# Kernel tuning notes

Measured on AMD Instinct MI355X. Metric: run time of the kernel, lower is better.

Reference implementation:

```python
import jax, jax.numpy as jnp
import numpy as np

WS = (7, 7)          # window size
N = WS[0] * WS[1]    # 49 tokens per window
C = 128              # dim
H = 4                # num heads
D = C // H           # head dim = 32
B = 8192             # batch * num_windows
NW = 1024            # windows per image
SCALE = D ** -0.5


def _relative_position_index():
    coords_h = np.arange(WS[0])
    coords_w = np.arange(WS[1])
    coords = np.stack(np.meshgrid(coords_h, coords_w, indexing='ij'))  # [2,Wh,Ww]
    flat = coords.reshape(2, -1)                                        # [2,N]
    rel = flat[:, :, None] - flat[:, None, :]                           # [2,N,N]
    rel = rel.transpose(1, 2, 0).astype(np.int64)                       # [N,N,2]
    rel[:, :, 0] += WS[0] - 1
    rel[:, :, 1] += WS[1] - 1
    rel[:, :, 0] *= 2 * WS[1] - 1
    return rel.sum(-1)                                                  # [N,N]


def setup_inputs() -> dict:
    key = jax.random.key(0)
    ks = jax.random.split(key, 8)
    s = 0.02
    return {
        'x': jax.random.normal(ks[0], (B, N, C), jnp.float32),
        'y': jax.random.normal(ks[1], (B, N, C), jnp.float32),
        'mask': jnp.zeros((NW, N, N), jnp.float32),
        'Wq': jax.random.normal(ks[2], (C, C), jnp.float32) * s,
        'bq': jnp.zeros((C,), jnp.float32),
        'Wkv': jax.random.normal(ks[3], (C, 2 * C), jnp.float32) * s,
        'bkv': jnp.zeros((2 * C,), jnp.float32),
        'bias_table': jax.random.normal(ks[4], ((2 * WS[0] - 1) * (2 * WS[1] - 1), H), jnp.float32) * s,
        'Wp': jax.random.normal(ks[5], (C, C), jnp.float32) * s,
        'bp': jnp.zeros((C,), jnp.float32),
        'rel_idx': jnp.asarray(_relative_position_index(), jnp.int32),
    }


def reference(x, y, mask, Wq, bq, Wkv, bkv, bias_table, Wp, bp, rel_idx):
    b = x.shape[0]
    # q/kv projections
    q = (x @ Wq + bq).reshape(b, N, H, D).transpose(0, 2, 1, 3) * SCALE   # [B,H,N,D]
    kv = (y @ Wkv + bkv).reshape(b, N, 2, H, D).transpose(2, 0, 3, 1, 4)  # [2,B,H,N,D]
    k, v = kv[0], kv[1]
    attn = jnp.einsum('bhnd,bhmd->bhnm', q, k)                            # [B,H,N,N]
    # relative position bias gather
    bias = bias_table[rel_idx.reshape(-1)].reshape(N, N, H).transpose(2, 0, 1)  # [H,N,N]
    attn = attn + bias[None]
    # mask add per window
    nW = mask.shape[0]
    attn = attn.reshape(b // nW, nW, H, N, N) + mask[None, :, None]
    attn = attn.reshape(b, H, N, N)
    attn = jax.nn.softmax(attn, axis=-1)
    out = jnp.einsum('bhnm,bhmd->bhnd', attn, v)                          # [B,H,N,D]
    out = out.transpose(0, 2, 1, 3).reshape(b, N, C)
    return out @ Wp + bp
```

## Files before the change

### kernel.cpp

```cpp
#include <hip/hip_runtime.h>
#include <cstddef>


#define MFMA16 __builtin_amdgcn_mfma_f32_16x16x32_bf16

typedef float f32x4 __attribute__((ext_vector_type(4)));
typedef __bf16 bf16x8 __attribute__((ext_vector_type(8)));
typedef unsigned short u16x8 __attribute__((ext_vector_type(8)));

constexpr int NTOK = 49;
constexpr int CDIM = 128;
constexpr int NWIN = 1024;
constexpr int NB = 8192;
constexpr float SCALE_F = 0.17677669529663687f;

__device__ __forceinline__ unsigned short f2bf(float f) {
  unsigned int u = __builtin_bit_cast(unsigned int, f);
  u += 0x7FFFu + ((u >> 16) & 1u);
  return (unsigned short)(u >> 16);
}

__device__ __forceinline__ int sw128(int row, int col) {
  return (row << 8) + ((((col >> 3) ^ row) & 15) << 4) + ((col & 7) << 1);
}
__device__ __forceinline__ int sw64(int row, int col) {
  return (row << 7) + ((((col >> 3) ^ (row >> 1)) & 7) << 4) + ((col & 7) << 1);
}

__global__ void prepack_kernel(const float* __restrict__ Wq, const float* __restrict__ Wkv,
                               const float* __restrict__ Wp, const float* __restrict__ bias_table,
                               const int* __restrict__ rel_idx,
                               unsigned short* __restrict__ wFrag, float* __restrict__ wBias) {
  int t = blockIdx.x * 256 + threadIdx.x;
  if (t < 8192) {
    const int mat = t >> 11;
    const int g = t & 2047;
    const int frag = g >> 6, lane = g & 63;
    const int nt = frag >> 2, ks = frag & 3;
    const int li = lane & 15, q4 = lane >> 4;
    const int n = nt * 16 + li;
    u16x8 tmp;
#pragma unroll
    for (int j = 0; j < 8; ++j) {
      const int k = ks * 32 + q4 * 8 + j;
      float v;
      if (mat == 0) v = Wq[k * 128 + n];
      else if (mat == 1) v = Wkv[k * 256 + n];
      else if (mat == 2) v = Wkv[k * 256 + 128 + n];
      else v = Wp[k * 128 + n];
      tmp[j] = f2bf(v);
    }
    *(u16x8*)(wFrag + (size_t)t * 8) = tmp;
  } else {
    const int tb = t - 8192;
    if (tb < 2401) {
      const int r = rel_idx[tb];
#pragma unroll
      for (int h = 0; h < 4; ++h) wBias[h * 2401 + tb] = bias_table[r * 4 + h];
    }
  }
}

__global__ __launch_bounds__(256, 3) void attn_kernel(
    const float* __restrict__ x, const float* __restrict__ y, const float* __restrict__ mask,
    const float* __restrict__ bq, const float* __restrict__ bkv, const float* __restrict__ bp,
    const unsigned short* __restrict__ wFrag, const float* __restrict__ wBias,
    float* __restrict__ out) {
  __shared__ __align__(16) unsigned char lds[49152];
  const int tid = threadIdx.x;
  const int w = tid >> 6;
  const int lane = tid & 63;
  const int li = lane & 15;
  const int q4 = lane >> 4;
  const int b = blockIdx.x;
  const int mh = w >> 1;
  const int nh = w & 1;

  bf16x8 ax[2][4], ay[2][4];
#pragma unroll
  for (int t = 0; t < 2; ++t) {
    const int mrow = mh * 32 + t * 16 + li;
    const bool mv = mrow < NTOK;
    const float* xr = x + ((size_t)b * NTOK + (mv ? mrow : 0)) * CDIM;
    const float* yr = y + ((size_t)b * NTOK + (mv ? mrow : 0)) * CDIM;
#pragma unroll
    for (int ks = 0; ks < 4; ++ks) {
      const int c0 = ks * 32 + q4 * 8;
      float4 a0 = *(const float4*)(xr + c0);
      float4 a1 = *(const float4*)(xr + c0 + 4);
      float4 b0 = *(const float4*)(yr + c0);
      float4 b1 = *(const float4*)(yr + c0 + 4);
      if (!mv) {
        a0.x = a0.y = a0.z = a0.w = 0.f; a1.x = a1.y = a1.z = a1.w = 0.f;
        b0.x = b0.y = b0.z = b0.w = 0.f; b1.x = b1.y = b1.z = b1.w = 0.f;
      }
      u16x8 ta, tb;
      ta[0] = f2bf(a0.x); ta[1] = f2bf(a0.y); ta[2] = f2bf(a0.z); ta[3] = f2bf(a0.w);
      ta[4] = f2bf(a1.x); ta[5] = f2bf(a1.y); ta[6] = f2bf(a1.z); ta[7] = f2bf(a1.w);
      tb[0] = f2bf(b0.x); tb[1] = f2bf(b0.y); tb[2] = f2bf(b0.z); tb[3] = f2bf(b0.w);
      tb[4] = f2bf(b1.x); tb[5] = f2bf(b1.y); tb[6] = f2bf(b1.z); tb[7] = f2bf(b1.w);
      ax[t][ks] = __builtin_bit_cast(bf16x8, ta);
      ay[t][ks] = __builtin_bit_cast(bf16x8, tb);
    }
  }

  const unsigned short* wq = wFrag + 0 * 16384 + nh * 8192;
  const unsigned short* wk = wFrag + 1 * 16384 + nh * 8192;
  const unsigned short* wv = wFrag + 2 * 16384 + nh * 8192;
  const unsigned short* wp = wFrag + 3 * 16384 + nh * 8192;

#pragma unroll
  for (int ntl = 0; ntl < 4; ++ntl) {
    bf16x8 wf[4];
#pragma unroll
    for (int ks = 0; ks < 4; ++ks)
      wf[ks] = *(const bf16x8*)(wq + (ntl * 4 + ks) * 512 + lane * 8);
    const int n = nh * 64 + ntl * 16 + li;
    const float bv = bq[n];
#pragma unroll
    for (int t = 0; t < 2; ++t) {
      f32x4 acc = {0.f, 0.f, 0.f, 0.f};
#pragma unroll
      for (int ks = 0; ks < 4; ++ks) acc = MFMA16(ax[t][ks], wf[ks], acc, 0, 0, 0);
#pragma unroll
      for (int r = 0; r < 4; ++r) {
        const int m = mh * 32 + t * 16 + q4 * 4 + r;
        *(unsigned short*)(lds + sw128(m, n)) = f2bf(acc[r] + bv);
      }
    }
  }
#pragma unroll
  for (int ntl = 0; ntl < 4; ++ntl) {
    bf16x8 wf[4];
#pragma unroll
    for (int ks = 0; ks < 4; ++ks)
      wf[ks] = *(const bf16x8*)(wk + (ntl * 4 + ks) * 512 + lane * 8);
    const int n = nh * 64 + ntl * 16 + li;
    const float bv = bkv[n];
#pragma unroll
    for (int t = 0; t < 2; ++t) {
      f32x4 acc = {0.f, 0.f, 0.f, 0.f};
#pragma unroll
      for (int ks = 0; ks < 4; ++ks) acc = MFMA16(ay[t][ks], wf[ks], acc, 0, 0, 0);
#pragma unroll
      for (int r = 0; r < 4; ++r) {
        const int m = mh * 32 + t * 16 + q4 * 4 + r;
        *(unsigned short*)(lds + 16384 + sw128(m, n)) = f2bf(acc[r] + bv);
      }
    }
  }
#pragma unroll
  for (int ntl = 0; ntl < 4; ++ntl) {
    bf16x8 wf[4];
#pragma unroll
    for (int ks = 0; ks < 4; ++ks)
      wf[ks] = *(const bf16x8*)(wv + (ntl * 4 + ks) * 512 + lane * 8);
    const int n = nh * 64 + ntl * 16 + li;
    const float bv = bkv[128 + n];
#pragma unroll
    for (int t = 0; t < 2; ++t) {
      f32x4 acc = {0.f, 0.f, 0.f, 0.f};
#pragma unroll
      for (int ks = 0; ks < 4; ++ks) acc = MFMA16(ay[t][ks], wf[ks], acc, 0, 0, 0);
#pragma unroll
      for (int r = 0; r < 4; ++r) {
        const int m = mh * 32 + t * 16 + q4 * 4 + r;
        *(unsigned short*)(lds + 32768 + sw64(n, m)) = f2bf(acc[r] + bv);
      }
    }
  }
  __syncthreads();

  const int h = w;
  const int PS = h * 8192;
  f32x4 s[4][4];
  {
    bf16x8 aq[4], bk[4];
#pragma unroll
    for (int mt = 0; mt < 4; ++mt)
      aq[mt] = *(const bf16x8*)(lds + sw128(mt * 16 + li, h * 32 + q4 * 8));
#pragma unroll
    for (int nt = 0; nt < 4; ++nt)
      bk[nt] = *(const bf16x8*)(lds + 16384 + sw128(nt * 16 + li, h * 32 + q4 * 8));
    const f32x4 zz = {0.f, 0.f, 0.f, 0.f};
#pragma unroll
    for (int mt = 0; mt < 4; ++mt)
#pragma unroll
      for (int nt = 0; nt < 4; ++nt) s[mt][nt] = MFMA16(aq[mt], bk[nt], zz, 0, 0, 0);
  }
  const float* __restrict__ maskw = mask + (size_t)(b & (NWIN - 1)) * 2401;
  const float* __restrict__ biash = wBias + h * 2401;
#pragma unroll
  for (int mt = 0; mt < 4; ++mt) {
#pragma unroll
    for (int r = 0; r < 4; ++r) {
      const int m = mt * 16 + q4 * 4 + r;
      const bool mvld = m < NTOK;
      const int mo = (mvld ? m : 0) * NTOK;
      float vv[4];
#pragma unroll
      for (int nt = 0; nt < 4; ++nt) {
        const int n = nt * 16 + li;
        float t = SCALE_F * s[mt][nt][r];
        if (n < NTOK) {
          if (mvld) t += biash[mo + n] + maskw[mo + n];
        } else {
          t = -1e30f;
        }
        vv[nt] = t;
      }
      float mx = fmaxf(fmaxf(vv[0], vv[1]), fmaxf(vv[2], vv[3]));
      mx = fmaxf(mx, __shfl_xor(mx, 1, 16));
      mx = fmaxf(mx, __shfl_xor(mx, 2, 16));
      mx = fmaxf(mx, __shfl_xor(mx, 4, 16));
      mx = fmaxf(mx, __shfl_xor(mx, 8, 16));
      float sm = 0.f;
#pragma unroll
      for (int nt = 0; nt < 4; ++nt) {
        vv[nt] = __expf(vv[nt] - mx);
        sm += vv[nt];
      }
      sm += __shfl_xor(sm, 1, 16);
      sm += __shfl_xor(sm, 2, 16);
      sm += __shfl_xor(sm, 4, 16);
      sm += __shfl_xor(sm, 8, 16);
      const float inv = __builtin_amdgcn_rcpf(sm);
#pragma unroll
      for (int nt = 0; nt < 4; ++nt) s[mt][nt][r] = vv[nt] * inv;
    }
  }
  __syncthreads();
#pragma unroll
  for (int mt = 0; mt < 4; ++mt)
#pragma unroll
    for (int r = 0; r < 4; ++r) {
      const int m = mt * 16 + q4 * 4 + r;
#pragma unroll
      for (int nt = 0; nt < 4; ++nt)
        *(unsigned short*)(lds + PS + sw64(m, nt * 16 + li)) = f2bf(s[mt][nt][r]);
    }

  f32x4 o[4][2];
  {
    bf16x8 ap[4][2], bv2[2][2];
#pragma unroll
    for (int mt = 0; mt < 4; ++mt)
#pragma unroll
      for (int ks = 0; ks < 2; ++ks)
        ap[mt][ks] = *(const bf16x8*)(lds + PS + sw64(mt * 16 + li, ks * 32 + q4 * 8));
#pragma unroll
    for (int nti = 0; nti < 2; ++nti)
#pragma unroll
      for (int ks = 0; ks < 2; ++ks)
        bv2[nti][ks] =
            *(const bf16x8*)(lds + 32768 + sw64(h * 32 + nti * 16 + li, ks * 32 + q4 * 8));
#pragma unroll
    for (int mt = 0; mt < 4; ++mt)
#pragma unroll
      for (int nti = 0; nti < 2; ++nti) {
        f32x4 acc = {0.f, 0.f, 0.f, 0.f};
#pragma unroll
        for (int ks = 0; ks < 2; ++ks) acc = MFMA16(ap[mt][ks], bv2[nti][ks], acc, 0, 0, 0);
        o[mt][nti] = acc;
      }
  }
  __syncthreads();

#pragma unroll
  for (int mt = 0; mt < 4; ++mt)
#pragma unroll
    for (int nti = 0; nti < 2; ++nti)
#pragma unroll
      for (int r = 0; r < 4; ++r) {
        const int m = mt * 16 + q4 * 4 + r;
        const int c = h * 32 + nti * 16 + li;
        *(unsigned short*)(lds + sw128(m, c)) = f2bf(o[mt][nti][r]);
      }
  __syncthreads();

  bf16x8 az[2][4];
#pragma unroll
  for (int t = 0; t < 2; ++t)
#pragma unroll
    for (int ks = 0; ks < 4; ++ks)
      az[t][ks] = *(const bf16x8*)(lds + sw128(mh * 32 + t * 16 + li, ks * 32 + q4 * 8));
#pragma unroll
  for (int ntl = 0; ntl < 4; ++ntl) {
    bf16x8 wf[4];
#pragma unroll
    for (int ks = 0; ks < 4; ++ks)
      wf[ks] = *(const bf16x8*)(wp + (ntl * 4 + ks) * 512 + lane * 8);
    const int n = nh * 64 + ntl * 16 + li;
    const float bpv = bp[n];
#pragma unroll
    for (int t = 0; t < 2; ++t) {
      f32x4 acc = {0.f, 0.f, 0.f, 0.f};
#pragma unroll
      for (int ks = 0; ks < 4; ++ks) acc = MFMA16(az[t][ks], wf[ks], acc, 0, 0, 0);
#pragma unroll
      for (int r = 0; r < 4; ++r) {
        const int m = mh * 32 + t * 16 + q4 * 4 + r;
        if (m < NTOK) out[((size_t)b * NTOK + m) * CDIM + n] = acc[r] + bpv;
      }
    }
  }
}

extern "C" void kernel_launch(void* const* d_in, const int* in_sizes, int n_in, void* d_out,
                              int out_size, void* d_ws, size_t ws_size, hipStream_t stream) {
  const float* x = (const float*)d_in[0];
  const float* y = (const float*)d_in[1];
  const float* mask = (const float*)d_in[2];
  const float* Wq = (const float*)d_in[3];
  const float* bq = (const float*)d_in[4];
  const float* Wkv = (const float*)d_in[5];
  const float* bkv = (const float*)d_in[6];
  const float* bt = (const float*)d_in[7];
  const float* Wp = (const float*)d_in[8];
  const float* bp = (const float*)d_in[9];
  const int* rel = (const int*)d_in[10];
  float* out = (float*)d_out;

  unsigned short* wFrag = (unsigned short*)d_ws;
  float* wBias = (float*)((char*)d_ws + 131072);

  prepack_kernel<<<64, 256, 0, stream>>>(Wq, Wkv, Wp, bt, rel, wFrag, wBias);
  attn_kernel<<<NB, 256, 0, stream>>>(x, y, mask, bq, bkv, bp, wFrag, wBias, out);
}
```

Baseline: 754.8 us.

## Transpose MFMA operands, cut LDS to 32KB, defer softmax normalization, vectorize stores

The kernel swaps MFMA operand order so each lane holds four consecutive channels or keys. That allows vectorized bf16x4 LDS writes and float4 output stores, and makes the softmax reduction mostly in-lane. LDS is cut from 48KB to 32KB by keeping V in registers until after QK^T, then reusing the K region. The P tile is staged in two halves per wave, with launch bounds raised to 4 blocks per SM. Softmax normalization is deferred to the output, and a pre-transposed mask and bias copy is made for coalesced reads. The costs are an extra mask-transpose kernel per call, more register pressure, and extra barriers.

```diff
diff --git a/kernel.cpp b/kernel.cpp
--- a/kernel.cpp
+++ b/kernel.cpp
@@ -6,7 +6,8 @@
 
 typedef float f32x4 __attribute__((ext_vector_type(4)));
 typedef __bf16 bf16x8 __attribute__((ext_vector_type(8)));
-typedef unsigned short u16x8 __attribute__((ext_vector_type(8)));
+typedef __bf16 bf16x4 __attribute__((ext_vector_type(4)));
+typedef __bf16 bf16x2 __attribute__((ext_vector_type(2)));
 
 constexpr int NTOK = 49;
 constexpr int CDIM = 128;
@@ -14,23 +15,20 @@
 constexpr int NB = 8192;
 constexpr float SCALE_F = 0.17677669529663687f;
 
-__device__ __forceinline__ unsigned short f2bf(float f) {
-  unsigned int u = __builtin_bit_cast(unsigned int, f);
-  u += 0x7FFFu + ((u >> 16) & 1u);
-  return (unsigned short)(u >> 16);
-}
-
 __device__ __forceinline__ int sw128(int row, int col) {
   return (row << 8) + ((((col >> 3) ^ row) & 15) << 4) + ((col & 7) << 1);
 }
 __device__ __forceinline__ int sw64(int row, int col) {
   return (row << 7) + ((((col >> 3) ^ (row >> 1)) & 7) << 4) + ((col & 7) << 1);
+}
+__device__ __forceinline__ int swp(int m, int nl) {
+  return (m << 6) + ((((nl >> 3) ^ (m >> 1)) & 3) << 4) + ((nl & 7) << 1);
 }
 
 __global__ void prepack_kernel(const float* __restrict__ Wq, const float* __restrict__ Wkv,
                                const float* __restrict__ Wp, const float* __restrict__ bias_table,
                                const int* __restrict__ rel_idx,
-                               unsigned short* __restrict__ wFrag, float* __restrict__ wBias) {
+                               unsigned short* __restrict__ wFrag, float* __restrict__ wBiasT) {
   int t = blockIdx.x * 256 + threadIdx.x;
   if (t < 8192) {
     const int mat = t >> 11;
@@ -39,7 +37,7 @@
     const int nt = frag >> 2, ks = frag & 3;
     const int li = lane & 15, q4 = lane >> 4;
     const int n = nt * 16 + li;
-    u16x8 tmp;
+    bf16x8 tmp;
 #pragma unroll
     for (int j = 0; j < 8; ++j) {
       const int k = ks * 32 + q4 * 8 + j;
@@ -48,25 +46,36 @@
       else if (mat == 1) v = Wkv[k * 256 + n];
       else if (mat == 2) v = Wkv[k * 256 + 128 + n];
       else v = Wp[k * 128 + n];
-      tmp[j] = f2bf(v);
-    }
-    *(u16x8*)(wFrag + (size_t)t * 8) = tmp;
+      tmp[j] = (__bf16)v;
+    }
+    *(bf16x8*)(wFrag + (size_t)t * 8) = tmp;
   } else {
     const int tb = t - 8192;
     if (tb < 2401) {
-      const int r = rel_idx[tb];
-#pragma unroll
-      for (int h = 0; h < 4; ++h) wBias[h * 2401 + tb] = bias_table[r * 4 + h];
-    }
-  }
-}
-
-__global__ __launch_bounds__(256, 3) void attn_kernel(
-    const float* __restrict__ x, const float* __restrict__ y, const float* __restrict__ mask,
+      const int m = tb % 49, n = tb / 49;
+      const int r = rel_idx[m * 49 + n];
+#pragma unroll
+      for (int h = 0; h < 4; ++h) wBiasT[h * 2401 + tb] = bias_table[r * 4 + h];
+    }
+  }
+}
+
+__global__ void maskT_kernel(const float* __restrict__ mask, float* __restrict__ maskT) {
+  const int w = blockIdx.x;
+  const float* src = mask + (size_t)w * 2401;
+  float* dst = maskT + (size_t)w * 2401;
+  for (int i = threadIdx.x; i < 2401; i += 256) {
+    dst[i] = src[(i % 49) * 49 + (i / 49)];
+  }
+}
+
+template <bool MASKT>
+__global__ __launch_bounds__(256, 4) void attn_kernel(
+    const float* __restrict__ x, const float* __restrict__ y, const float* __restrict__ maskp,
     const float* __restrict__ bq, const float* __restrict__ bkv, const float* __restrict__ bp,
-    const unsigned short* __restrict__ wFrag, const float* __restrict__ wBias,
+    const unsigned short* __restrict__ wFrag, const float* __restrict__ wBiasT,
     float* __restrict__ out) {
-  __shared__ __align__(16) unsigned char lds[49152];
+  __shared__ __align__(16) unsigned char lds[32768];
   const int tid = threadIdx.x;
   const int w = tid >> 6;
   const int lane = tid & 63;
@@ -94,13 +103,13 @@
         a0.x = a0.y = a0.z = a0.w = 0.f; a1.x = a1.y = a1.z = a1.w = 0.f;
         b0.x = b0.y = b0.z = b0.w = 0.f; b1.x = b1.y = b1.z = b1.w = 0.f;
       }
-      u16x8 ta, tb;
-      ta[0] = f2bf(a0.x); ta[1] = f2bf(a0.y); ta[2] = f2bf(a0.z); ta[3] = f2bf(a0.w);
-      ta[4] = f2bf(a1.x); ta[5] = f2bf(a1.y); ta[6] = f2bf(a1.z); ta[7] = f2bf(a1.w);
-      tb[0] = f2bf(b0.x); tb[1] = f2bf(b0.y); tb[2] = f2bf(b0.z); tb[3] = f2bf(b0.w);
-      tb[4] = f2bf(b1.x); tb[5] = f2bf(b1.y); tb[6] = f2bf(b1.z); tb[7] = f2bf(b1.w);
-      ax[t][ks] = __builtin_bit_cast(bf16x8, ta);
-      ay[t][ks] = __builtin_bit_cast(bf16x8, tb);
+      bf16x8 ta, tb;
+      ta[0] = (__bf16)a0.x; ta[1] = (__bf16)a0.y; ta[2] = (__bf16)a0.z; ta[3] = (__bf16)a0.w;
+      ta[4] = (__bf16)a1.x; ta[5] = (__bf16)a1.y; ta[6] = (__bf16)a1.z; ta[7] = (__bf16)a1.w;
+      tb[0] = (__bf16)b0.x; tb[1] = (__bf16)b0.y; tb[2] = (__bf16)b0.z; tb[3] = (__bf16)b0.w;
+      tb[4] = (__bf16)b1.x; tb[5] = (__bf16)b1.y; tb[6] = (__bf16)b1.z; tb[7] = (__bf16)b1.w;
+      ax[t][ks] = ta;
+      ay[t][ks] = tb;
     }
   }
 
@@ -113,169 +122,201 @@
   for (int ntl = 0; ntl < 4; ++ntl) {
     bf16x8 wf[4];
 #pragma unroll
-    for (int ks = 0; ks < 4; ++ks)
-      wf[ks] = *(const bf16x8*)(wq + (ntl * 4 + ks) * 512 + lane * 8);
-    const int n = nh * 64 + ntl * 16 + li;
-    const float bv = bq[n];
+    for (int ks = 0; ks < 4; ++ks) wf[ks] = *(const bf16x8*)(wq + (ntl * 4 + ks) * 512 + lane * 8);
+    const int ch0 = nh * 64 + ntl * 16 + q4 * 4;
+    const float4 b4 = *(const float4*)(bq + ch0);
 #pragma unroll
     for (int t = 0; t < 2; ++t) {
       f32x4 acc = {0.f, 0.f, 0.f, 0.f};
 #pragma unroll
-      for (int ks = 0; ks < 4; ++ks) acc = MFMA16(ax[t][ks], wf[ks], acc, 0, 0, 0);
-#pragma unroll
-      for (int r = 0; r < 4; ++r) {
-        const int m = mh * 32 + t * 16 + q4 * 4 + r;
-        *(unsigned short*)(lds + sw128(m, n)) = f2bf(acc[r] + bv);
-      }
+      for (int ks = 0; ks < 4; ++ks) acc = MFMA16(wf[ks], ax[t][ks], acc, 0, 0, 0);
+      const int tok = mh * 32 + t * 16 + li;
+      bf16x4 pv;
+      pv[0] = (__bf16)(acc[0] + b4.x); pv[1] = (__bf16)(acc[1] + b4.y);
+      pv[2] = (__bf16)(acc[2] + b4.z); pv[3] = (__bf16)(acc[3] + b4.w);
+      *(bf16x4*)(lds + sw128(tok, ch0)) = pv;
     }
   }
 #pragma unroll
   for (int ntl = 0; ntl < 4; ++ntl) {
     bf16x8 wf[4];
 #pragma unroll
-    for (int ks = 0; ks < 4; ++ks)
-      wf[ks] = *(const bf16x8*)(wk + (ntl * 4 + ks) * 512 + lane * 8);
-    const int n = nh * 64 + ntl * 16 + li;
-    const float bv = bkv[n];
+    for (int ks = 0; ks < 4; ++ks) wf[ks] = *(const bf16x8*)(wk + (ntl * 4 + ks) * 512 + lane * 8);
+    const int ch0 = nh * 64 + ntl * 16 + q4 * 4;
+    const float4 b4 = *(const float4*)(bkv + ch0);
 #pragma unroll
     for (int t = 0; t < 2; ++t) {
       f32x4 acc = {0.f, 0.f, 0.f, 0.f};
 #pragma unroll
+      for (int ks = 0; ks < 4; ++ks) acc = MFMA16(wf[ks], ay[t][ks], acc, 0, 0, 0);
+      const int tok = mh * 32 + t * 16 + li;
+      bf16x4 pv;
+      pv[0] = (__bf16)(acc[0] + b4.x); pv[1] = (__bf16)(acc[1] + b4.y);
+      pv[2] = (__bf16)(acc[2] + b4.z); pv[3] = (__bf16)(acc[3] + b4.w);
+      *(bf16x4*)(lds + 16384 + sw128(tok, ch0)) = pv;
+    }
+  }
+  bf16x2 vpk[2][4][2];
+#pragma unroll
+  for (int ntl = 0; ntl < 4; ++ntl) {
+    bf16x8 wf[4];
+#pragma unroll
+    for (int ks = 0; ks < 4; ++ks) wf[ks] = *(const bf16x8*)(wv + (ntl * 4 + ks) * 512 + lane * 8);
+    const int nV = nh * 64 + ntl * 16 + li;
+    const float bvv = bkv[128 + nV];
+#pragma unroll
+    for (int t = 0; t < 2; ++t) {
+      f32x4 acc = {0.f, 0.f, 0.f, 0.f};
+#pragma unroll
       for (int ks = 0; ks < 4; ++ks) acc = MFMA16(ay[t][ks], wf[ks], acc, 0, 0, 0);
-#pragma unroll
-      for (int r = 0; r < 4; ++r) {
-        const int m = mh * 32 + t * 16 + q4 * 4 + r;
-        *(unsigned short*)(lds + 16384 + sw128(m, n)) = f2bf(acc[r] + bv);
-      }
-    }
-  }
-#pragma unroll
-  for (int ntl = 0; ntl < 4; ++ntl) {
-    bf16x8 wf[4];
-#pragma unroll
-    for (int ks = 0; ks < 4; ++ks)
-      wf[ks] = *(const bf16x8*)(wv + (ntl * 4 + ks) * 512 + lane * 8);
-    const int n = nh * 64 + ntl * 16 + li;
-    const float bv = bkv[128 + n];
-#pragma unroll
-    for (int t = 0; t < 2; ++t) {
-      f32x4 acc = {0.f, 0.f, 0.f, 0.f};
-#pragma unroll
-      for (int ks = 0; ks < 4; ++ks) acc = MFMA16(ay[t][ks], wf[ks], acc, 0, 0, 0);
-#pragma unroll
-      for (int r = 0; r < 4; ++r) {
-        const int m = mh * 32 + t * 16 + q4 * 4 + r;
-        *(unsigned short*)(lds + 32768 + sw64(n, m)) = f2bf(acc[r] + bv);
-      }
+      vpk[t][ntl][0][0] = (__bf16)(acc[0] + bvv);
+      vpk[t][ntl][0][1] = (__bf16)(acc[1] + bvv);
+      vpk[t][ntl][1][0] = (__bf16)(acc[2] + bvv);
+      vpk[t][ntl][1][1] = (__bf16)(acc[3] + bvv);
     }
   }
   __syncthreads();
 
   const int h = w;
-  const int PS = h * 8192;
   f32x4 s[4][4];
   {
-    bf16x8 aq[4], bk[4];
+    bf16x8 aqf[4], bkf[4];
 #pragma unroll
     for (int mt = 0; mt < 4; ++mt)
-      aq[mt] = *(const bf16x8*)(lds + sw128(mt * 16 + li, h * 32 + q4 * 8));
-#pragma unroll
-    for (int nt = 0; nt < 4; ++nt)
-      bk[nt] = *(const bf16x8*)(lds + 16384 + sw128(nt * 16 + li, h * 32 + q4 * 8));
+      aqf[mt] = *(const bf16x8*)(lds + sw128(mt * 16 + li, h * 32 + q4 * 8));
+#pragma unroll
+    for (int nt = 0; nt < 4; ++nt)
+      bkf[nt] = *(const bf16x8*)(lds + 16384 + sw128(nt * 16 + li, h * 32 + q4 * 8));
     const f32x4 zz = {0.f, 0.f, 0.f, 0.f};
 #pragma unroll
+    for (int nt = 0; nt < 4; ++nt)
+#pragma unroll
+      for (int mt = 0; mt < 4; ++mt) s[nt][mt] = MFMA16(bkf[nt], aqf[mt], zz, 0, 0, 0);
+  }
+  __syncthreads();
+
+  unsigned char* const pbase = lds + w * 4096;
+#pragma unroll
+  for (int ntl = 0; ntl < 4; ++ntl) {
+    const int nV = nh * 64 + ntl * 16 + li;
+#pragma unroll
+    for (int t = 0; t < 2; ++t) {
+      const int m0 = mh * 32 + t * 16 + q4 * 4;
+      *(bf16x2*)(lds + 16384 + sw64(nV, m0)) = vpk[t][ntl][0];
+      *(bf16x2*)(lds + 16384 + sw64(nV, m0 + 2)) = vpk[t][ntl][1];
+    }
+  }
+
+  const float* __restrict__ maskw = maskp + (size_t)(b & (NWIN - 1)) * 2401;
+  const float* __restrict__ biash = wBiasT + h * 2401;
+  float inv[4];
+  bf16x2 pP[4][4][2];
+#pragma unroll
+  for (int mt = 0; mt < 4; ++mt) {
+    const int m = mt * 16 + li;
+    const int mm = m < NTOK ? m : 0;
+    float vv[4][4];
+#pragma unroll
+    for (int nt = 0; nt < 4; ++nt)
+#pragma unroll
+      for (int r = 0; r < 4; ++r) {
+        const int n = nt * 16 + q4 * 4 + r;
+        float tv = SCALE_F * s[nt][mt][r];
+        if (n < NTOK) {
+          if (MASKT) tv += biash[n * 49 + mm] + maskw[n * 49 + mm];
+          else       tv += biash[n * 49 + mm] + maskw[mm * 49 + n];
+        } else {
+          tv = -1e30f;
+        }
+        vv[nt][r] = tv;
+      }
+    float mx = vv[0][0];
+#pragma unroll
+    for (int nt = 0; nt < 4; ++nt)
+#pragma unroll
+      for (int r = 0; r < 4; ++r) mx = fmaxf(mx, vv[nt][r]);
+    mx = fmaxf(mx, __shfl_xor(mx, 16));
+    mx = fmaxf(mx, __shfl_xor(mx, 32));
+    float sm = 0.f;
+#pragma unroll
+    for (int nt = 0; nt < 4; ++nt)
+#pragma unroll
+      for (int r = 0; r < 4; ++r) {
+        const float e = __expf(vv[nt][r] - mx);
+        vv[nt][r] = e;
+        sm += e;
+      }
+    sm += __shfl_xor(sm, 16);
+    sm += __shfl_xor(sm, 32);
+    inv[mt] = __builtin_amdgcn_rcpf(sm);
+#pragma unroll
+    for (int nt = 0; nt < 4; ++nt) {
+      pP[nt][mt][0][0] = (__bf16)vv[nt][0];
+      pP[nt][mt][0][1] = (__bf16)vv[nt][1];
+      pP[nt][mt][1][0] = (__bf16)vv[nt][2];
+      pP[nt][mt][1][1] = (__bf16)vv[nt][3];
+    }
+  }
+#pragma unroll
+  for (int nt = 0; nt < 2; ++nt)
+#pragma unroll
+    for (int mt = 0; mt < 4; ++mt) {
+      bf16x4 pv;
+      pv[0] = pP[nt][mt][0][0]; pv[1] = pP[nt][mt][0][1];
+      pv[2] = pP[nt][mt][1][0]; pv[3] = pP[nt][mt][1][1];
+      *(bf16x4*)(pbase + swp(mt * 16 + li, nt * 16 + q4 * 4)) = pv;
+    }
+  __syncthreads();
+
+  bf16x8 bv2[2][2];
+#pragma unroll
+  for (int cht = 0; cht < 2; ++cht)
+#pragma unroll
+    for (int ksn = 0; ksn < 2; ++ksn)
+      bv2[cht][ksn] =
+          *(const bf16x8*)(lds + 16384 + sw64(h * 32 + cht * 16 + li, ksn * 32 + q4 * 8));
+  f32x4 o[2][4];
+  {
+    bf16x8 ap[4];
+#pragma unroll
     for (int mt = 0; mt < 4; ++mt)
-#pragma unroll
-      for (int nt = 0; nt < 4; ++nt) s[mt][nt] = MFMA16(aq[mt], bk[nt], zz, 0, 0, 0);
-  }
-  const float* __restrict__ maskw = mask + (size_t)(b & (NWIN - 1)) * 2401;
-  const float* __restrict__ biash = wBias + h * 2401;
-#pragma unroll
-  for (int mt = 0; mt < 4; ++mt) {
-#pragma unroll
-    for (int r = 0; r < 4; ++r) {
-      const int m = mt * 16 + q4 * 4 + r;
-      const bool mvld = m < NTOK;
-      const int mo = (mvld ? m : 0) * NTOK;
-      float vv[4];
-#pragma unroll
-      for (int nt = 0; nt < 4; ++nt) {
-        const int n = nt * 16 + li;
-        float t = SCALE_F * s[mt][nt][r];
-        if (n < NTOK) {
-          if (mvld) t += biash[mo + n] + maskw[mo + n];
-        } else {
-          t = -1e30f;
-        }
-        vv[nt] = t;
-      }
-      float mx = fmaxf(fmaxf(vv[0], vv[1]), fmaxf(vv[2], vv[3]));
-      mx = fmaxf(mx, __shfl_xor(mx, 1, 16));
-      mx = fmaxf(mx, __shfl_xor(mx, 2, 16));
-      mx = fmaxf(mx, __shfl_xor(mx, 4, 16));
-      mx = fmaxf(mx, __shfl_xor(mx, 8, 16));
-      float sm = 0.f;
-#pragma unroll
-      for (int nt = 0; nt < 4; ++nt) {
-        vv[nt] = __expf(vv[nt] - mx);
-        sm += vv[nt];
-      }
-      sm += __shfl_xor(sm, 1, 16);
-      sm += __shfl_xor(sm, 2, 16);
-      sm += __shfl_xor(sm, 4, 16);
-      sm += __shfl_xor(sm, 8, 16);
-      const float inv = __builtin_amdgcn_rcpf(sm);
-#pragma unroll
-      for (int nt = 0; nt < 4; ++nt) s[mt][nt][r] = vv[nt] * inv;
-    }
-  }
-  __syncthreads();
-#pragma unroll
-  for (int mt = 0; mt < 4; ++mt)
-#pragma unroll
-    for (int r = 0; r < 4; ++r) {
-      const int m = mt * 16 + q4 * 4 + r;
-#pragma unroll
-      for (int nt = 0; nt < 4; ++nt)
-        *(unsigned short*)(lds + PS + sw64(m, nt * 16 + li)) = f2bf(s[mt][nt][r]);
-    }
-
-  f32x4 o[4][2];
-  {
-    bf16x8 ap[4][2], bv2[2][2];
+      ap[mt] = *(const bf16x8*)(pbase + swp(mt * 16 + li, q4 * 8));
+    const f32x4 zz = {0.f, 0.f, 0.f, 0.f};
+#pragma unroll
+    for (int cht = 0; cht < 2; ++cht)
+#pragma unroll
+      for (int mt = 0; mt < 4; ++mt) o[cht][mt] = MFMA16(bv2[cht][0], ap[mt], zz, 0, 0, 0);
+#pragma unroll
+    for (int nt = 0; nt < 2; ++nt)
+#pragma unroll
+      for (int mt = 0; mt < 4; ++mt) {
+        bf16x4 pv;
+        pv[0] = pP[2 + nt][mt][0][0]; pv[1] = pP[2 + nt][mt][0][1];
+        pv[2] = pP[2 + nt][mt][1][0]; pv[3] = pP[2 + nt][mt][1][1];
+        *(bf16x4*)(pbase + swp(mt * 16 + li, nt * 16 + q4 * 4)) = pv;
+      }
 #pragma unroll
     for (int mt = 0; mt < 4; ++mt)
-#pragma unroll
-      for (int ks = 0; ks < 2; ++ks)
-        ap[mt][ks] = *(const bf16x8*)(lds + PS + sw64(mt * 16 + li, ks * 32 + q4 * 8));
-#pragma unroll
-    for (int nti = 0; nti < 2; ++nti)
-#pragma unroll
-      for (int ks = 0; ks < 2; ++ks)
-        bv2[nti][ks] =
-            *(const bf16x8*)(lds + 32768 + sw64(h * 32 + nti * 16 + li, ks * 32 + q4 * 8));
-#pragma unroll
-    for (int mt = 0; mt < 4; ++mt)
-#pragma unroll
-      for (int nti = 0; nti < 2; ++nti) {
-        f32x4 acc = {0.f, 0.f, 0.f, 0.f};
-#pragma unroll
-        for (int ks = 0; ks < 2; ++ks) acc = MFMA16(ap[mt][ks], bv2[nti][ks], acc, 0, 0, 0);
-        o[mt][nti] = acc;
-      }
-  }
-  __syncthreads();
-
-#pragma unroll
-  for (int mt = 0; mt < 4; ++mt)
-#pragma unroll
-    for (int nti = 0; nti < 2; ++nti)
-#pragma unroll
-      for (int r = 0; r < 4; ++r) {
-        const int m = mt * 16 + q4 * 4 + r;
-        const int c = h * 32 + nti * 16 + li;
-        *(unsigned short*)(lds + sw128(m, c)) = f2bf(o[mt][nti][r]);
-      }
+      ap[mt] = *(const bf16x8*)(pbase + swp(mt * 16 + li, q4 * 8));
+#pragma unroll
+    for (int cht = 0; cht < 2; ++cht)
+#pragma unroll
+      for (int mt = 0; mt < 4; ++mt)
+        o[cht][mt] = MFMA16(bv2[cht][1], ap[mt], o[cht][mt], 0, 0, 0);
+  }
+  __syncthreads();
+
+#pragma unroll
+  for (int cht = 0; cht < 2; ++cht)
+#pragma unroll
+    for (int mt = 0; mt < 4; ++mt) {
+      bf16x4 zv;
+      zv[0] = (__bf16)(o[cht][mt][0] * inv[mt]);
+      zv[1] = (__bf16)(o[cht][mt][1] * inv[mt]);
+      zv[2] = (__bf16)(o[cht][mt][2] * inv[mt]);
+      zv[3] = (__bf16)(o[cht][mt][3] * inv[mt]);
+      *(bf16x4*)(lds + sw128(mt * 16 + li, h * 32 + cht * 16 + q4 * 4)) = zv;
+    }
   __syncthreads();
 
   bf16x8 az[2][4];
@@ -288,19 +329,20 @@
   for (int ntl = 0; ntl < 4; ++ntl) {
     bf16x8 wf[4];
 #pragma unroll
-    for (int ks = 0; ks < 4; ++ks)
-      wf[ks] = *(const bf16x8*)(wp + (ntl * 4 + ks) * 512 + lane * 8);
-    const int n = nh * 64 + ntl * 16 + li;
-    const float bpv = bp[n];
+    for (int ks = 0; ks < 4; ++ks) wf[ks] = *(const bf16x8*)(wp + (ntl * 4 + ks) * 512 + lane * 8);
+    const int ch0 = nh * 64 + ntl * 16 + q4 * 4;
+    const float4 b4 = *(const float4*)(bp + ch0);
 #pragma unroll
     for (int t = 0; t < 2; ++t) {
       f32x4 acc = {0.f, 0.f, 0.f, 0.f};
 #pragma unroll
-      for (int ks = 0; ks < 4; ++ks) acc = MFMA16(az[t][ks], wf[ks], acc, 0, 0, 0);
-#pragma unroll
-      for (int r = 0; r < 4; ++r) {
-        const int m = mh * 32 + t * 16 + q4 * 4 + r;
-        if (m < NTOK) out[((size_t)b * NTOK + m) * CDIM + n] = acc[r] + bpv;
+      for (int ks = 0; ks < 4; ++ks) acc = MFMA16(wf[ks], az[t][ks], acc, 0, 0, 0);
+      const int tok = mh * 32 + t * 16 + li;
+      if (tok < NTOK) {
+        float4 st;
+        st.x = acc[0] + b4.x; st.y = acc[1] + b4.y;
+        st.z = acc[2] + b4.z; st.w = acc[3] + b4.w;
+        *(float4*)(out + ((size_t)b * NTOK + tok) * CDIM + ch0) = st;
       }
     }
   }
@@ -322,8 +364,15 @@
   float* out = (float*)d_out;
 
   unsigned short* wFrag = (unsigned short*)d_ws;
-  float* wBias = (float*)((char*)d_ws + 131072);
-
-  prepack_kernel<<<64, 256, 0, stream>>>(Wq, Wkv, Wp, bt, rel, wFrag, wBias);
-  attn_kernel<<<NB, 256, 0, stream>>>(x, y, mask, bq, bkv, bp, wFrag, wBias, out);
-}
+  float* wBiasT = (float*)((char*)d_ws + 131072);
+  float* maskT = (float*)((char*)d_ws + 196608);
+  const size_t needT = 196608 + (size_t)NWIN * 2401 * sizeof(float);
+
+  prepack_kernel<<<64, 256, 0, stream>>>(Wq, Wkv, Wp, bt, rel, wFrag, wBiasT);
+  if (ws_size >= needT) {
+    maskT_kernel<<<NWIN, 256, 0, stream>>>(mask, maskT);
+    attn_kernel<true><<<NB, 256, 0, stream>>>(x, y, maskT, bq, bkv, bp, wFrag, wBiasT, out);
+  } else {
+    attn_kernel<false><<<NB, 256, 0, stream>>>(x, y, mask, bq, bkv, bp, wFrag, wBiasT, out);
+  }
+}
```

Result: faster. 683.5 us (-9.5%).
